# Optimization experiments

Hardware: AMD Instinct MI355X
Metric: run time of the kernel (lower is better)

Reference implementation:

```python
import jax, jax.numpy as jnp
import numpy as np

LEVEL = 3  # matches init_kwargs
# pywt Wavelet('db4').rec_lo (synthesis low-pass, 8 taps)
REC_LO = np.array([
    0.23037781330885523, 0.7148465705525415, 0.6308807679295904,
    -0.02798376941698385, -0.18703481171888114, 0.030841381835986965,
    0.032883011666982945, -0.010597401784997278], dtype=np.float32)


def _rec_filters():
    rec_lo = jnp.asarray(REC_LO)
    L = rec_lo.shape[0]
    # QMF relation: rec_hi[k] = (-1)^k * rec_lo[L-1-k]
    signs = jnp.asarray((-1.0) ** np.arange(L), dtype=rec_lo.dtype)
    rec_hi = rec_lo[::-1] * signs
    return rec_lo, rec_hi


def _iswt(coeffs, rec_lo, rec_hi):
    """Inverse stationary (undecimated / a-trous) wavelet transform.

    coeffs = [cA_L, cD_L, cD_{L-1}, ..., cD_1], each of shape [BN, T].
    Perfect reconstruction for the circular-padded dilated-conv SWT
    (ptwt/pywt convention): at each level with dilation d,
      x[n] = 0.5 * sum_m rec_lo[m]*a[(n - d*(m - L//2 + 1)) % T]
                 + rec_hi[m]*cd[(n - d*(m - L//2 + 1)) % T]
    """
    L = rec_lo.shape[0]
    n_lev = len(coeffs) - 1
    res = coeffs[0]
    for c_pos in range(n_lev):
        hi = coeffs[1 + c_pos]
        d = 2 ** (n_lev - 1 - c_pos)
        acc = jnp.zeros_like(res)
        for m in range(L):  # static 8-tap loop, unrolled under jit
            shift = d * (m - L // 2 + 1)
            acc = acc + rec_lo[m] * jnp.roll(res, shift, axis=-1) \
                      + rec_hi[m] * jnp.roll(hi, shift, axis=-1)
        res = 0.5 * acc
    return res


def setup_inputs() -> dict:
    key = jax.random.key(0)
    B, N, T = 32, 64, 4096
    x = jax.random.normal(key, (B, (LEVEL + 1) * N, T), dtype=jnp.float32)
    return {"x": x}


def reference(x):
    B, expanded_N, T = x.shape
    N = expanded_N // (LEVEL + 1)
    xr = x.reshape(B * N, LEVEL + 1, T)  # (B,N,level+1,T) merged over B,N
    coeffs = [xr[:, i, :] for i in range(LEVEL + 1)]
    rec_lo, rec_hi = _rec_filters()
    rec = _iswt(coeffs, rec_lo, rec_hi)  # [B*N, T]
    return rec.reshape(B, N, T)
```

## Files before the change

### kernel.cpp

```cpp
#include <hip/hip_runtime.h>


namespace {

constexpr int TT = 4096;
constexpr int T4 = TT / 4;
constexpr int NT = 512;
constexpr int NCH = 2;

#define GLD16(gp, lp)                                                      \
  __builtin_amdgcn_global_load_lds(                                        \
      (const __attribute__((address_space(1))) void*)(gp),                 \
      (__attribute__((address_space(3))) void*)(lp), 16, 0, 0)

__device__ __forceinline__ int sl(int c) {
  c &= (T4 - 1);
  return c ^ ((c >> 3) & 7);
}

template <int D>
__device__ __forceinline__ void level_compute(const float* lds_res,
                                              const float* lds_hi, int u,
                                              float4 acc[NCH]) {
  constexpr float LO[8] = {
      0.23037781330885523f,  0.7148465705525415f,  0.6308807679295904f,
      -0.02798376941698385f, -0.18703481171888114f, 0.030841381835986965f,
      0.032883011666982945f, -0.010597401784997278f};
  constexpr float HI[8] = {
      -0.010597401784997278f, -0.032883011666982945f, 0.030841381835986965f,
      0.18703481171888114f,   -0.02798376941698385f,  -0.6308807679295904f,
      0.7148465705525415f,    -0.23037781330885523f};

  constexpr int W4 = (7 * D + 4 * NCH + 3) / 4;
  const float4* res4 = reinterpret_cast<const float4*>(lds_res);
  const float4* hir4 = reinterpret_cast<const float4*>(lds_hi);
  const int c0 = NCH * u - D;

  float w[4 * W4];
  float a[NCH][4];

#pragma unroll
  for (int i = 0; i < W4; ++i) {
    const float4 v = res4[sl(c0 + i)];
    w[4 * i + 0] = v.x; w[4 * i + 1] = v.y;
    w[4 * i + 2] = v.z; w[4 * i + 3] = v.w;
  }
#pragma unroll
  for (int jc = 0; jc < NCH; ++jc)
#pragma unroll
    for (int r = 0; r < 4; ++r) a[jc][r] = 0.f;
#pragma unroll
  for (int m = 0; m < 8; ++m) {
    const int o = D * (7 - m);
#pragma unroll
    for (int jc = 0; jc < NCH; ++jc)
#pragma unroll
      for (int r = 0; r < 4; ++r) a[jc][r] += LO[m] * w[o + 4 * jc + r];
  }

#pragma unroll
  for (int i = 0; i < W4; ++i) {
    const float4 v = hir4[sl(c0 + i)];
    w[4 * i + 0] = v.x; w[4 * i + 1] = v.y;
    w[4 * i + 2] = v.z; w[4 * i + 3] = v.w;
  }
#pragma unroll
  for (int m = 0; m < 8; ++m) {
    const int o = D * (7 - m);
#pragma unroll
    for (int jc = 0; jc < NCH; ++jc)
#pragma unroll
      for (int r = 0; r < 4; ++r) a[jc][r] += HI[m] * w[o + 4 * jc + r];
  }

#pragma unroll
  for (int jc = 0; jc < NCH; ++jc)
    acc[jc] = make_float4(0.5f * a[jc][0], 0.5f * a[jc][1],
                          0.5f * a[jc][2], 0.5f * a[jc][3]);
}

__global__ __launch_bounds__(NT, 4) void iswt_kernel(const float* __restrict__ x,
                                                     float* __restrict__ out) {
  __shared__ __align__(16) float lds_res[TT];
  __shared__ __align__(16) float lds_h3[TT];
  __shared__ __align__(16) float lds_h2[TT];
  __shared__ __align__(16) float lds_h1[TT];

  const int t = threadIdx.x;
  const int row = blockIdx.x;

  const float* xr = x + (size_t)row * 4 * TT;

#pragma unroll
  for (int k = 0; k < NCH; ++k) {
    const int s = k * NT + t;
    GLD16(xr + 0 * TT + sl(s) * 4, lds_res + s * 4);
  }
#pragma unroll
  for (int k = 0; k < NCH; ++k) {
    const int s = k * NT + t;
    GLD16(xr + 1 * TT + sl(s) * 4, lds_h3 + s * 4);
  }
#pragma unroll
  for (int k = 0; k < NCH; ++k) {
    const int s = k * NT + t;
    GLD16(xr + 2 * TT + sl(s) * 4, lds_h2 + s * 4);
  }
#pragma unroll
  for (int k = 0; k < NCH; ++k) {
    const int s = k * NT + t;
    GLD16(xr + 3 * TT + sl(s) * 4, lds_h1 + s * 4);
  }

  float4* res4 = reinterpret_cast<float4*>(lds_res);
  float4 acc[NCH];

  asm volatile("s_waitcnt vmcnt(4)\n\ts_barrier" ::: "memory");

  level_compute<4>(lds_res, lds_h3, t, acc);
  asm volatile("s_waitcnt lgkmcnt(0)\n\ts_barrier" ::: "memory");
#pragma unroll
  for (int jc = 0; jc < NCH; ++jc) res4[sl(NCH * t + jc)] = acc[jc];
  asm volatile("s_waitcnt vmcnt(2) lgkmcnt(0)\n\ts_barrier" ::: "memory");

  level_compute<2>(lds_res, lds_h2, t, acc);
  asm volatile("s_waitcnt lgkmcnt(0)\n\ts_barrier" ::: "memory");
#pragma unroll
  for (int jc = 0; jc < NCH; ++jc) res4[sl(NCH * t + jc)] = acc[jc];
  asm volatile("s_waitcnt vmcnt(0) lgkmcnt(0)\n\ts_barrier" ::: "memory");

  level_compute<1>(lds_res, lds_h1, t, acc);

  float4* bounce4 = reinterpret_cast<float4*>(lds_h3);
#pragma unroll
  for (int jc = 0; jc < NCH; ++jc) bounce4[sl(NCH * t + jc)] = acc[jc];
  asm volatile("s_waitcnt lgkmcnt(0)\n\ts_barrier" ::: "memory");

  float4* out4 = reinterpret_cast<float4*>(out) + (size_t)row * T4;
#pragma unroll
  for (int k = 0; k < NCH; ++k) {
    const int c = k * NT + t;
    out4[c] = bounce4[sl(c)];
  }
}

}

extern "C" void kernel_launch(void* const* d_in, const int* in_sizes, int n_in,
                              void* d_out, int out_size, void* d_ws, size_t ws_size,
                              hipStream_t stream) {
  const float* x = reinterpret_cast<const float*>(d_in[0]);
  float* out = reinterpret_cast<float*>(d_out);
  const int rows = out_size / TT;
  iswt_kernel<<<rows, NT, 0, stream>>>(x, out);
}
```

Before: 196.7 us.

## Collapse three ISWT levels into single composite convolution filters per input

Precomputes, at compile time, composite filters that map cA and each detail band directly to the final output: 50-tap for cA and cD3, 22-tap for cD2, and 8-tap for cD1. This removes the intermediate LDS writes and reads and the barriers between levels, and the output is written straight from registers instead of through an LDS bounce. In exchange it does more FMAs per output (about 130 taps vs 48), needs a 60-float register window, and the sums are reordered, which can shift float rounding slightly.

```diff
diff --git a/kernel.cpp b/kernel.cpp
--- a/kernel.cpp
+++ b/kernel.cpp
@@ -6,7 +6,41 @@
 constexpr int TT = 4096;
 constexpr int T4 = TT / 4;
 constexpr int NT = 512;
-constexpr int NCH = 2;
+
+struct Filters {
+  float fa[50];
+  float fd3[50];
+  float fd2[22];
+  float fd1[8];
+};
+
+constexpr Filters make_filters() {
+  const double lo[8] = {
+      0.23037781330885523,  0.7148465705525415,  0.6308807679295904,
+      -0.02798376941698385, -0.18703481171888114, 0.030841381835986965,
+      0.032883011666982945, -0.010597401784997278};
+  double hi[8] = {};
+  for (int m = 0; m < 8; ++m) hi[m] = ((m & 1) ? -1.0 : 1.0) * lo[7 - m];
+
+  double fa[50] = {}, fd3[50] = {}, fd2[22] = {};
+  for (int m1 = 0; m1 < 8; ++m1)
+    for (int m2 = 0; m2 < 8; ++m2)
+      for (int m3 = 0; m3 < 8; ++m3) {
+        const int s = 4 * (m1 - 3) + 2 * (m2 - 3) + (m3 - 3);
+        fa[s + 21]  += 0.125 * lo[m1] * lo[m2] * lo[m3];
+        fd3[s + 21] += 0.125 * hi[m1] * lo[m2] * lo[m3];
+      }
+  for (int m2 = 0; m2 < 8; ++m2)
+    for (int m3 = 0; m3 < 8; ++m3)
+      fd2[2 * (m2 - 3) + (m3 - 3) + 9] += 0.25 * hi[m2] * lo[m3];
+
+  Filters f{};
+  for (int i = 0; i < 50; ++i) { f.fa[i] = (float)fa[i]; f.fd3[i] = (float)fd3[i]; }
+  for (int i = 0; i < 22; ++i) f.fd2[i] = (float)fd2[i];
+  for (int m = 0; m < 8; ++m) f.fd1[m] = (float)(0.5 * hi[m]);
+  return f;
+}
+constexpr Filters F = make_filters();
 
 #define GLD16(gp, lp)                                                      \
   __builtin_amdgcn_global_load_lds(                                        \
@@ -18,70 +52,9 @@
   return c ^ ((c >> 3) & 7);
 }
 
-template <int D>
-__device__ __forceinline__ void level_compute(const float* lds_res,
-                                              const float* lds_hi, int u,
-                                              float4 acc[NCH]) {
-  constexpr float LO[8] = {
-      0.23037781330885523f,  0.7148465705525415f,  0.6308807679295904f,
-      -0.02798376941698385f, -0.18703481171888114f, 0.030841381835986965f,
-      0.032883011666982945f, -0.010597401784997278f};
-  constexpr float HI[8] = {
-      -0.010597401784997278f, -0.032883011666982945f, 0.030841381835986965f,
-      0.18703481171888114f,   -0.02798376941698385f,  -0.6308807679295904f,
-      0.7148465705525415f,    -0.23037781330885523f};
-
-  constexpr int W4 = (7 * D + 4 * NCH + 3) / 4;
-  const float4* res4 = reinterpret_cast<const float4*>(lds_res);
-  const float4* hir4 = reinterpret_cast<const float4*>(lds_hi);
-  const int c0 = NCH * u - D;
-
-  float w[4 * W4];
-  float a[NCH][4];
-
-#pragma unroll
-  for (int i = 0; i < W4; ++i) {
-    const float4 v = res4[sl(c0 + i)];
-    w[4 * i + 0] = v.x; w[4 * i + 1] = v.y;
-    w[4 * i + 2] = v.z; w[4 * i + 3] = v.w;
-  }
-#pragma unroll
-  for (int jc = 0; jc < NCH; ++jc)
-#pragma unroll
-    for (int r = 0; r < 4; ++r) a[jc][r] = 0.f;
-#pragma unroll
-  for (int m = 0; m < 8; ++m) {
-    const int o = D * (7 - m);
-#pragma unroll
-    for (int jc = 0; jc < NCH; ++jc)
-#pragma unroll
-      for (int r = 0; r < 4; ++r) a[jc][r] += LO[m] * w[o + 4 * jc + r];
-  }
-
-#pragma unroll
-  for (int i = 0; i < W4; ++i) {
-    const float4 v = hir4[sl(c0 + i)];
-    w[4 * i + 0] = v.x; w[4 * i + 1] = v.y;
-    w[4 * i + 2] = v.z; w[4 * i + 3] = v.w;
-  }
-#pragma unroll
-  for (int m = 0; m < 8; ++m) {
-    const int o = D * (7 - m);
-#pragma unroll
-    for (int jc = 0; jc < NCH; ++jc)
-#pragma unroll
-      for (int r = 0; r < 4; ++r) a[jc][r] += HI[m] * w[o + 4 * jc + r];
-  }
-
-#pragma unroll
-  for (int jc = 0; jc < NCH; ++jc)
-    acc[jc] = make_float4(0.5f * a[jc][0], 0.5f * a[jc][1],
-                          0.5f * a[jc][2], 0.5f * a[jc][3]);
-}
-
 __global__ __launch_bounds__(NT, 4) void iswt_kernel(const float* __restrict__ x,
                                                      float* __restrict__ out) {
-  __shared__ __align__(16) float lds_res[TT];
+  __shared__ __align__(16) float lds_cA[TT];
   __shared__ __align__(16) float lds_h3[TT];
   __shared__ __align__(16) float lds_h2[TT];
   __shared__ __align__(16) float lds_h1[TT];
@@ -92,56 +65,97 @@
   const float* xr = x + (size_t)row * 4 * TT;
 
 #pragma unroll
-  for (int k = 0; k < NCH; ++k) {
+  for (int k = 0; k < 2; ++k) {
     const int s = k * NT + t;
-    GLD16(xr + 0 * TT + sl(s) * 4, lds_res + s * 4);
+    GLD16(xr + 0 * TT + sl(s) * 4, lds_cA + s * 4);
   }
 #pragma unroll
-  for (int k = 0; k < NCH; ++k) {
+  for (int k = 0; k < 2; ++k) {
     const int s = k * NT + t;
     GLD16(xr + 1 * TT + sl(s) * 4, lds_h3 + s * 4);
   }
 #pragma unroll
-  for (int k = 0; k < NCH; ++k) {
+  for (int k = 0; k < 2; ++k) {
     const int s = k * NT + t;
     GLD16(xr + 2 * TT + sl(s) * 4, lds_h2 + s * 4);
   }
 #pragma unroll
-  for (int k = 0; k < NCH; ++k) {
+  for (int k = 0; k < 2; ++k) {
     const int s = k * NT + t;
     GLD16(xr + 3 * TT + sl(s) * 4, lds_h1 + s * 4);
   }
 
-  float4* res4 = reinterpret_cast<float4*>(lds_res);
-  float4 acc[NCH];
+  float acc[8];
+#pragma unroll
+  for (int j = 0; j < 8; ++j) acc[j] = 0.f;
+
+  float w[60];
 
   asm volatile("s_waitcnt vmcnt(4)\n\ts_barrier" ::: "memory");
 
-  level_compute<4>(lds_res, lds_h3, t, acc);
-  asm volatile("s_waitcnt lgkmcnt(0)\n\ts_barrier" ::: "memory");
+  const float4* cA4 = reinterpret_cast<const float4*>(lds_cA);
+  const float4* h34 = reinterpret_cast<const float4*>(lds_h3);
+  const float4* h24 = reinterpret_cast<const float4*>(lds_h2);
+  const float4* h14 = reinterpret_cast<const float4*>(lds_h1);
+
+  const int c0 = 2 * t - 7;
 #pragma unroll
-  for (int jc = 0; jc < NCH; ++jc) res4[sl(NCH * t + jc)] = acc[jc];
-  asm volatile("s_waitcnt vmcnt(2) lgkmcnt(0)\n\ts_barrier" ::: "memory");
+  for (int i = 0; i < 15; ++i) {
+    const float4 v = cA4[sl(c0 + i)];
+    w[4 * i + 0] = v.x; w[4 * i + 1] = v.y;
+    w[4 * i + 2] = v.z; w[4 * i + 3] = v.w;
+  }
+#pragma unroll
+  for (int ia = 0; ia < 50; ++ia) {
+    const float f = F.fa[ia];
+#pragma unroll
+    for (int j = 0; j < 8; ++j) acc[j] += f * w[j + 49 - ia];
+  }
 
-  level_compute<2>(lds_res, lds_h2, t, acc);
-  asm volatile("s_waitcnt lgkmcnt(0)\n\ts_barrier" ::: "memory");
 #pragma unroll
-  for (int jc = 0; jc < NCH; ++jc) res4[sl(NCH * t + jc)] = acc[jc];
-  asm volatile("s_waitcnt vmcnt(0) lgkmcnt(0)\n\ts_barrier" ::: "memory");
+  for (int i = 0; i < 15; ++i) {
+    const float4 v = h34[sl(c0 + i)];
+    w[4 * i + 0] = v.x; w[4 * i + 1] = v.y;
+    w[4 * i + 2] = v.z; w[4 * i + 3] = v.w;
+  }
+#pragma unroll
+  for (int ia = 0; ia < 50; ++ia) {
+    const float f = F.fd3[ia];
+#pragma unroll
+    for (int j = 0; j < 8; ++j) acc[j] += f * w[j + 49 - ia];
+  }
 
-  level_compute<1>(lds_res, lds_h1, t, acc);
+  asm volatile("s_waitcnt vmcnt(0)\n\ts_barrier" ::: "memory");
 
-  float4* bounce4 = reinterpret_cast<float4*>(lds_h3);
 #pragma unroll
-  for (int jc = 0; jc < NCH; ++jc) bounce4[sl(NCH * t + jc)] = acc[jc];
-  asm volatile("s_waitcnt lgkmcnt(0)\n\ts_barrier" ::: "memory");
+  for (int i = 0; i < 8; ++i) {
+    const float4 v = h24[sl(2 * t - 3 + i)];
+    w[4 * i + 0] = v.x; w[4 * i + 1] = v.y;
+    w[4 * i + 2] = v.z; w[4 * i + 3] = v.w;
+  }
+#pragma unroll
+  for (int ia = 0; ia < 22; ++ia) {
+    const float f = F.fd2[ia];
+#pragma unroll
+    for (int j = 0; j < 8; ++j) acc[j] += f * w[j + 21 - ia];
+  }
+
+#pragma unroll
+  for (int i = 0; i < 4; ++i) {
+    const float4 v = h14[sl(2 * t - 1 + i)];
+    w[4 * i + 0] = v.x; w[4 * i + 1] = v.y;
+    w[4 * i + 2] = v.z; w[4 * i + 3] = v.w;
+  }
+#pragma unroll
+  for (int ia = 0; ia < 8; ++ia) {
+    const float f = F.fd1[ia];
+#pragma unroll
+    for (int j = 0; j < 8; ++j) acc[j] += f * w[j + 7 - ia];
+  }
 
   float4* out4 = reinterpret_cast<float4*>(out) + (size_t)row * T4;
-#pragma unroll
-  for (int k = 0; k < NCH; ++k) {
-    const int c = k * NT + t;
-    out4[c] = bounce4[sl(c)];
-  }
+  out4[2 * t + 0] = make_float4(acc[0], acc[1], acc[2], acc[3]);
+  out4[2 * t + 1] = make_float4(acc[4], acc[5], acc[6], acc[7]);
 }
 
 }
```

Measured after the change: 200.9 us. 1.02x slower.

## Process four rows per block with double-buffered LDS prefetch and register-held detail coeffs

Applied to the files above, without the earlier changes.

Each block now handles four consecutive rows. The cA and cD3 planes of the next row are prefetched into a second LDS buffer pair while the current row computes. The cD2 and cD1 planes are no longer staged in LDS; each thread loads its halo window straight from global memory into registers. The final output is written directly from registers instead of going through an LDS bounce. This cuts LDS footprint and LDS traffic and overlaps loads with compute, but the grid shrinks fourfold (512 blocks), which may reduce parallelism across CUs and adds redundant global reads for the halos.

```diff
diff --git a/kernel.cpp b/kernel.cpp
--- a/kernel.cpp
+++ b/kernel.cpp
@@ -6,7 +6,16 @@
 constexpr int TT = 4096;
 constexpr int T4 = TT / 4;
 constexpr int NT = 512;
-constexpr int NCH = 2;
+constexpr int R  = 4;
+
+constexpr float LO[8] = {
+    0.23037781330885523f,  0.7148465705525415f,  0.6308807679295904f,
+    -0.02798376941698385f, -0.18703481171888114f, 0.030841381835986965f,
+    0.032883011666982945f, -0.010597401784997278f};
+constexpr float HI[8] = {
+    -0.010597401784997278f, -0.032883011666982945f, 0.030841381835986965f,
+    0.18703481171888114f,   -0.02798376941698385f,  -0.6308807679295904f,
+    0.7148465705525415f,    -0.23037781330885523f};
 
 #define GLD16(gp, lp)                                                      \
   __builtin_amdgcn_global_load_lds(                                        \
@@ -18,130 +27,149 @@
   return c ^ ((c >> 3) & 7);
 }
 
-template <int D>
-__device__ __forceinline__ void level_compute(const float* lds_res,
-                                              const float* lds_hi, int u,
-                                              float4 acc[NCH]) {
-  constexpr float LO[8] = {
-      0.23037781330885523f,  0.7148465705525415f,  0.6308807679295904f,
-      -0.02798376941698385f, -0.18703481171888114f, 0.030841381835986965f,
-      0.032883011666982945f, -0.010597401784997278f};
-  constexpr float HI[8] = {
-      -0.010597401784997278f, -0.032883011666982945f, 0.030841381835986965f,
-      0.18703481171888114f,   -0.02798376941698385f,  -0.6308807679295904f,
-      0.7148465705525415f,    -0.23037781330885523f};
-
-  constexpr int W4 = (7 * D + 4 * NCH + 3) / 4;
-  const float4* res4 = reinterpret_cast<const float4*>(lds_res);
-  const float4* hir4 = reinterpret_cast<const float4*>(lds_hi);
-  const int c0 = NCH * u - D;
-
-  float w[4 * W4];
-  float a[NCH][4];
-
+template <int W4>
+__device__ __forceinline__ void lds_window(const float4* b, int c0, float* w) {
 #pragma unroll
   for (int i = 0; i < W4; ++i) {
-    const float4 v = res4[sl(c0 + i)];
+    const float4 v = b[sl(c0 + i)];
     w[4 * i + 0] = v.x; w[4 * i + 1] = v.y;
     w[4 * i + 2] = v.z; w[4 * i + 3] = v.w;
   }
+}
+
+template <int NC>
+__device__ __forceinline__ void reg_window(const float4* d, float* w) {
 #pragma unroll
-  for (int jc = 0; jc < NCH; ++jc)
-#pragma unroll
-    for (int r = 0; r < 4; ++r) a[jc][r] = 0.f;
+  for (int i = 0; i < NC; ++i) {
+    w[4 * i + 0] = d[i].x; w[4 * i + 1] = d[i].y;
+    w[4 * i + 2] = d[i].z; w[4 * i + 3] = d[i].w;
+  }
+}
+
+template <int D>
+__device__ __forceinline__ void accum(const float* c, const float* w,
+                                      float a[2][4]) {
 #pragma unroll
   for (int m = 0; m < 8; ++m) {
     const int o = D * (7 - m);
 #pragma unroll
-    for (int jc = 0; jc < NCH; ++jc)
+    for (int jc = 0; jc < 2; ++jc)
 #pragma unroll
-      for (int r = 0; r < 4; ++r) a[jc][r] += LO[m] * w[o + 4 * jc + r];
+      for (int r = 0; r < 4; ++r) a[jc][r] += c[m] * w[o + 4 * jc + r];
   }
+}
+
+template <int VMC, bool PREF>
+__device__ __forceinline__ void do_row(const float* xrow, const float* xnext,
+                                       float* Pc, float* Qc, float* Pn,
+                                       float* Qn, float* outrow, int t) {
+  const float4* P4 = reinterpret_cast<const float4*>(Pc);
+  const float4* Q4 = reinterpret_cast<const float4*>(Qc);
+  float4* Pw = reinterpret_cast<float4*>(Pc);
+
+  asm volatile("s_waitcnt lgkmcnt(0)\n\ts_barrier" ::: "memory");
+  if constexpr (PREF) {
+#pragma unroll
+    for (int k = 0; k < 2; ++k) {
+      const int s = k * NT + t;
+      GLD16(xnext + 0 * TT + sl(s) * 4, Pn + s * 4);
+    }
+#pragma unroll
+    for (int k = 0; k < 2; ++k) {
+      const int s = k * NT + t;
+      GLD16(xnext + 1 * TT + sl(s) * 4, Qn + s * 4);
+    }
+  }
+  asm volatile("s_waitcnt vmcnt(%0)\n\ts_barrier" ::"n"(VMC) : "memory");
+
+  const float4* g2 = reinterpret_cast<const float4*>(xrow + 2 * TT);
+  const float4* g1 = reinterpret_cast<const float4*>(xrow + 3 * TT);
+  float4 d2[6], d1[4];
+#pragma unroll
+  for (int i = 0; i < 6; ++i) d2[i] = g2[(2 * t - 2 + i) & (T4 - 1)];
+#pragma unroll
+  for (int i = 0; i < 4; ++i) d1[i] = g1[(2 * t - 1 + i) & (T4 - 1)];
+
+  float w[36];
+  float a[2][4] = {{0.f, 0.f, 0.f, 0.f}, {0.f, 0.f, 0.f, 0.f}};
+
+  lds_window<9>(P4, 2 * t - 4, w);
+  accum<4>(LO, w, a);
+  lds_window<9>(Q4, 2 * t - 4, w);
+  accum<4>(HI, w, a);
+  float4 r0 = make_float4(0.5f * a[0][0], 0.5f * a[0][1], 0.5f * a[0][2],
+                          0.5f * a[0][3]);
+  float4 r1 = make_float4(0.5f * a[1][0], 0.5f * a[1][1], 0.5f * a[1][2],
+                          0.5f * a[1][3]);
+
+  asm volatile("s_waitcnt lgkmcnt(0)\n\ts_barrier" ::: "memory");
+  Pw[sl(2 * t)] = r0;
+  Pw[sl(2 * t + 1)] = r1;
+  asm volatile("s_waitcnt lgkmcnt(0)\n\ts_barrier" ::: "memory");
 
 #pragma unroll
-  for (int i = 0; i < W4; ++i) {
-    const float4 v = hir4[sl(c0 + i)];
-    w[4 * i + 0] = v.x; w[4 * i + 1] = v.y;
-    w[4 * i + 2] = v.z; w[4 * i + 3] = v.w;
-  }
+  for (int jc = 0; jc < 2; ++jc)
 #pragma unroll
-  for (int m = 0; m < 8; ++m) {
-    const int o = D * (7 - m);
-#pragma unroll
-    for (int jc = 0; jc < NCH; ++jc)
-#pragma unroll
-      for (int r = 0; r < 4; ++r) a[jc][r] += HI[m] * w[o + 4 * jc + r];
-  }
+    for (int r = 0; r < 4; ++r) a[jc][r] = 0.f;
+  lds_window<6>(P4, 2 * t - 2, w);
+  accum<2>(LO, w, a);
+  reg_window<6>(d2, w);
+  accum<2>(HI, w, a);
+  r0 = make_float4(0.5f * a[0][0], 0.5f * a[0][1], 0.5f * a[0][2],
+                   0.5f * a[0][3]);
+  r1 = make_float4(0.5f * a[1][0], 0.5f * a[1][1], 0.5f * a[1][2],
+                   0.5f * a[1][3]);
+
+  asm volatile("s_waitcnt lgkmcnt(0)\n\ts_barrier" ::: "memory");
+  Pw[sl(2 * t)] = r0;
+  Pw[sl(2 * t + 1)] = r1;
+  asm volatile("s_waitcnt lgkmcnt(0)\n\ts_barrier" ::: "memory");
 
 #pragma unroll
-  for (int jc = 0; jc < NCH; ++jc)
-    acc[jc] = make_float4(0.5f * a[jc][0], 0.5f * a[jc][1],
-                          0.5f * a[jc][2], 0.5f * a[jc][3]);
+  for (int jc = 0; jc < 2; ++jc)
+#pragma unroll
+    for (int r = 0; r < 4; ++r) a[jc][r] = 0.f;
+  lds_window<4>(P4, 2 * t - 1, w);
+  accum<1>(LO, w, a);
+  reg_window<4>(d1, w);
+  accum<1>(HI, w, a);
+
+  float4* out4 = reinterpret_cast<float4*>(outrow);
+  out4[2 * t + 0] = make_float4(0.5f * a[0][0], 0.5f * a[0][1],
+                                0.5f * a[0][2], 0.5f * a[0][3]);
+  out4[2 * t + 1] = make_float4(0.5f * a[1][0], 0.5f * a[1][1],
+                                0.5f * a[1][2], 0.5f * a[1][3]);
 }
 
 __global__ __launch_bounds__(NT, 4) void iswt_kernel(const float* __restrict__ x,
                                                      float* __restrict__ out) {
-  __shared__ __align__(16) float lds_res[TT];
-  __shared__ __align__(16) float lds_h3[TT];
-  __shared__ __align__(16) float lds_h2[TT];
-  __shared__ __align__(16) float lds_h1[TT];
+  __shared__ __align__(16) float P0[TT], Q0[TT], P1[TT], Q1[TT];
 
   const int t = threadIdx.x;
-  const int row = blockIdx.x;
+  const size_t blk = blockIdx.x;
 
-  const float* xr = x + (size_t)row * 4 * TT;
+  const float* xg = x + blk * (size_t)(R * 4 * TT);
+  float* og = out + blk * (size_t)(R * TT);
 
 #pragma unroll
-  for (int k = 0; k < NCH; ++k) {
+  for (int k = 0; k < 2; ++k) {
     const int s = k * NT + t;
-    GLD16(xr + 0 * TT + sl(s) * 4, lds_res + s * 4);
+    GLD16(xg + 0 * TT + sl(s) * 4, P0 + s * 4);
   }
 #pragma unroll
-  for (int k = 0; k < NCH; ++k) {
+  for (int k = 0; k < 2; ++k) {
     const int s = k * NT + t;
-    GLD16(xr + 1 * TT + sl(s) * 4, lds_h3 + s * 4);
-  }
-#pragma unroll
-  for (int k = 0; k < NCH; ++k) {
-    const int s = k * NT + t;
-    GLD16(xr + 2 * TT + sl(s) * 4, lds_h2 + s * 4);
-  }
-#pragma unroll
-  for (int k = 0; k < NCH; ++k) {
-    const int s = k * NT + t;
-    GLD16(xr + 3 * TT + sl(s) * 4, lds_h1 + s * 4);
+    GLD16(xg + 1 * TT + sl(s) * 4, Q0 + s * 4);
   }
 
-  float4* res4 = reinterpret_cast<float4*>(lds_res);
-  float4 acc[NCH];
-
-  asm volatile("s_waitcnt vmcnt(4)\n\ts_barrier" ::: "memory");
-
-  level_compute<4>(lds_res, lds_h3, t, acc);
-  asm volatile("s_waitcnt lgkmcnt(0)\n\ts_barrier" ::: "memory");
-#pragma unroll
-  for (int jc = 0; jc < NCH; ++jc) res4[sl(NCH * t + jc)] = acc[jc];
-  asm volatile("s_waitcnt vmcnt(2) lgkmcnt(0)\n\ts_barrier" ::: "memory");
-
-  level_compute<2>(lds_res, lds_h2, t, acc);
-  asm volatile("s_waitcnt lgkmcnt(0)\n\ts_barrier" ::: "memory");
-#pragma unroll
-  for (int jc = 0; jc < NCH; ++jc) res4[sl(NCH * t + jc)] = acc[jc];
-  asm volatile("s_waitcnt vmcnt(0) lgkmcnt(0)\n\ts_barrier" ::: "memory");
-
-  level_compute<1>(lds_res, lds_h1, t, acc);
-
-  float4* bounce4 = reinterpret_cast<float4*>(lds_h3);
-#pragma unroll
-  for (int jc = 0; jc < NCH; ++jc) bounce4[sl(NCH * t + jc)] = acc[jc];
-  asm volatile("s_waitcnt lgkmcnt(0)\n\ts_barrier" ::: "memory");
-
-  float4* out4 = reinterpret_cast<float4*>(out) + (size_t)row * T4;
-#pragma unroll
-  for (int k = 0; k < NCH; ++k) {
-    const int c = k * NT + t;
-    out4[c] = bounce4[sl(c)];
-  }
+  do_row<4,  true >(xg + 0 * 4 * TT, xg + 1 * 4 * TT, P0, Q0, P1, Q1,
+                    og + 0 * TT, t);
+  do_row<18, true >(xg + 1 * 4 * TT, xg + 2 * 4 * TT, P1, Q1, P0, Q0,
+                    og + 1 * TT, t);
+  do_row<18, true >(xg + 2 * 4 * TT, xg + 3 * 4 * TT, P0, Q0, P1, Q1,
+                    og + 2 * TT, t);
+  do_row<14, false>(xg + 3 * 4 * TT, nullptr,          P1, Q1, P0, Q0,
+                    og + 3 * TT, t);
 }
 
 }
@@ -152,5 +180,5 @@
   const float* x = reinterpret_cast<const float*>(d_in[0]);
   float* out = reinterpret_cast<float*>(d_out);
   const int rows = out_size / TT;
-  iswt_kernel<<<rows, NT, 0, stream>>>(x, out);
+  iswt_kernel<<<rows / R, NT, 0, stream>>>(x, out);
 }
```

New measurement: 198.3 us. No clear change (+0.8%).
